# Kernel tuning notes

Hardware: AMD Instinct MI355X
Metric: run time of the kernel (lower is better)

## Reference

```python
import jax, jax.numpy as jnp
import numpy as np

N_NODES = 20000
N_EDGES = 320000
F_IN = 128
H = 4        # heads per layer
D = 128      # per-head hidden dim
NEG_SLOPE = 0.2


def setup_inputs() -> dict:
    key = jax.random.key(0)
    ks = jax.random.split(key, 14)
    s = 0.05
    inp = {
        "feats": jax.random.normal(ks[0], (N_NODES, F_IN), jnp.float32),
        "src": jax.random.randint(ks[1], (N_EDGES,), 0, N_NODES, jnp.int64),
        "dst": jax.random.randint(ks[2], (N_EDGES,), 0, N_NODES, jnp.int64),
        # layer 1: in F_IN -> H heads x D, flatten agg
        "W1": s * jax.random.normal(ks[3], (F_IN, H * D), jnp.float32),
        "al1": s * jax.random.normal(ks[4], (H, D), jnp.float32),
        "ar1": s * jax.random.normal(ks[5], (H, D), jnp.float32),
        "b1": jnp.zeros((H * D,), jnp.float32),
        # layer 2: in H*D -> H heads x D, mean agg
        "W2": s * jax.random.normal(ks[6], (H * D, H * D), jnp.float32),
        "al2": s * jax.random.normal(ks[7], (H, D), jnp.float32),
        "ar2": s * jax.random.normal(ks[8], (H, D), jnp.float32),
        "b2": jnp.zeros((H * D,), jnp.float32),
        # readout Linear(D, 1)
        "Wr": s * jax.random.normal(ks[9], (D, 1), jnp.float32),
        "br": jnp.zeros((1,), jnp.float32),
    }
    return inp


def _gat_conv(x, src, dst, W, al, ar, b, n_nodes):
    """dgl GATConv: per-head linear, edge softmax over incoming edges, scatter-sum."""
    h, d = al.shape
    z = (x @ W).reshape(n_nodes, h, d)                      # [N,H,D]
    el = jnp.einsum('nhd,hd->nh', z, al)                    # [N,H]
    er = jnp.einsum('nhd,hd->nh', z, ar)                    # [N,H]
    e = jax.nn.leaky_relu(el[src] + er[dst], NEG_SLOPE)     # [E,H]
    # numerically stable softmax grouped by destination node
    emax = jax.lax.stop_gradient(jax.ops.segment_max(e, dst, num_segments=n_nodes))
    a = jnp.exp(e - emax[dst])                              # [E,H]
    denom = jax.ops.segment_sum(a, dst, num_segments=n_nodes)
    alpha = a / jnp.maximum(denom[dst], 1e-9)               # [E,H]
    out = jax.ops.segment_sum(alpha[:, :, None] * z[src], dst, num_segments=n_nodes)
    return out + b.reshape(1, h, d)                         # [N,H,D]


def reference(feats, src, dst, W1, al1, ar1, b1, W2, al2, ar2, b2, Wr, br):
    n = feats.shape[0]
    h1 = _gat_conv(feats, src, dst, W1, al1, ar1, b1, n)    # [N,H,D]
    h1 = jax.nn.elu(h1.reshape(n, -1))                      # flatten heads -> [N,H*D]
    h2 = _gat_conv(h1, src, dst, W2, al2, ar2, b2, n)       # [N,H,D]
    h2 = h2.mean(axis=1)                                    # mean over heads -> [N,D]
    node_preds = h2 @ Wr + br                               # [N,1]
    return node_preds.sum(axis=0)                           # [1]
```

## Files before the change

### kernel.cpp

```cpp
#include <hip/hip_runtime.h>
#include <hip/hip_bf16.h>
#include <cstddef>

constexpr int NN = 20000;
constexpr int NE = 320000;
constexpr int NHEAD = 4;
constexpr int ND = 128;
constexpr int HD = 512;
constexpr int MPAD = 20096;
constexpr int SLOTS = 64;
constexpr float NEG_SLOPE = 0.2f;

using short8 = __attribute__((ext_vector_type(8))) short;
using f32x4 = __attribute__((ext_vector_type(4))) float;
using f32x2 = __attribute__((ext_vector_type(2))) float;

__device__ inline void gload16(const void* g, void* l) {
  __builtin_amdgcn_global_load_lds(
      (const __attribute__((address_space(1))) void*)g,
      (__attribute__((address_space(3))) void*)l, 16, 0, 0);
}

__device__ inline unsigned char f32_to_fp8(float v) {
  int pk = __builtin_amdgcn_cvt_pk_fp8_f32(v, v, 0, false);
  return (unsigned char)(pk & 0xff);
}

__device__ inline float fastrcp(float x) { return __builtin_amdgcn_rcpf(x); }

__device__ inline float fast_elu(float x) {
  return (x > 0.f) ? x : (__expf(x) - 1.0f);
}

constexpr int S0 = NN;
constexpr int S1 = S0 + MPAD * 128 / 4;
constexpr int S2 = S1 + 512 * 128;
constexpr int S3 = S2 + 12 * 512;
constexpr int S4 = S3 + 256;
__global__ __launch_bounds__(256) void prep_kernel(
    const float* __restrict__ feats, const float* __restrict__ W1,
    const float* __restrict__ W2, const float* __restrict__ al2,
    const float* __restrict__ ar2, const float* __restrict__ Wr,
    __hip_bfloat16* __restrict__ featsb, __hip_bfloat16* __restrict__ W1t,
    float* __restrict__ vcomb, float* __restrict__ partials,
    int* __restrict__ cnt) {
  int t = blockIdx.x * 256 + threadIdx.x;
  if (t < S0) {
    cnt[t] = 0;
  } else if (t < S1) {
    int u = (t - S0) * 4;
    float4 f = (u < NN * 128) ? *reinterpret_cast<const float4*>(&feats[u])
                              : make_float4(0.f, 0.f, 0.f, 0.f);
    __hip_bfloat162 o0 = __float22bfloat162_rn(make_float2(f.x, f.y));
    __hip_bfloat162 o1 = __float22bfloat162_rn(make_float2(f.z, f.w));
    uint2 pk;
    pk.x = *reinterpret_cast<unsigned int*>(&o0);
    pk.y = *reinterpret_cast<unsigned int*>(&o1);
    *reinterpret_cast<uint2*>(&featsb[u]) = pk;
  } else if (t < S2) {
    int u = t - S1;
    W1t[u] = __float2bfloat16(W1[(size_t)(u & 127) * 512 + (u >> 7)]);
  } else if (t < S3) {
    int u = t - S2;
    int v = u >> 9, k = u & 511;
    int h = (v < 4) ? v : (v < 8) ? v - 4 : v - 8;
    const float* vec = (v < 4) ? (al2 + h * 128)
                     : (v < 8) ? (ar2 + h * 128) : Wr;
    const float* wrow = W2 + (size_t)k * 512 + h * 128;
    float s = 0.f;
    for (int d = 0; d < 128; ++d) s += wrow[d] * vec[d];
    vcomb[u] = s;
  } else if (t < S4) {
    partials[t - S3] = 0.f;
  }
}

__global__ __launch_bounds__(256) void gemm1_kernel(
    const __hip_bfloat16* __restrict__ A,
    const __hip_bfloat16* __restrict__ Bt,
    unsigned char* __restrict__ C,
    const float* __restrict__ al, const float* __restrict__ ar,
    float* __restrict__ el, float* __restrict__ er,
    const int* __restrict__ src, const int* __restrict__ dst,
    int* __restrict__ cnt, int* __restrict__ src_perm) {
  constexpr int K = 128;
  __shared__ short As[128 * 32];
  __shared__ short Bs[128 * 32];
  __shared__ float elbuf[4][128];
  __shared__ float erbuf[4][128];
  int t = threadIdx.x;

  {
    int nth = gridDim.x * gridDim.y * 256;
    int gid = (blockIdx.y * gridDim.x + blockIdx.x) * 256 + t;
    for (int e = gid; e < NE; e += nth) {
      int d = dst[e];
      int p = atomicAdd(&cnt[d], 1);
      if (p < SLOTS) src_perm[d * SLOTS + p] = src[e];
    }
  }

  int lane = t & 63;
  int wave = t >> 6;
  int rowBase = blockIdx.x * 128;
  int head = blockIdx.y;
  int colBase = head * 128;
  int woffr = (wave & 1) * 64;
  int woffc = (wave >> 1) * 64;
  int mrow = lane & 15, quad = lane >> 4;

  f32x4 acc[4][4];
#pragma unroll
  for (int i = 0; i < 4; ++i)
#pragma unroll
    for (int j = 0; j < 4; ++j) acc[i][j] = (f32x4){0.f, 0.f, 0.f, 0.f};

  for (int k0 = 0; k0 < K; k0 += 32) {
#pragma unroll
    for (int p = 0; p < 2; ++p) {
      int f = p * 256 + wave * 64 + lane;
      int r = f >> 2, kc = f & 3;
      gload16(A + (size_t)(rowBase + r) * K + k0 + kc * 8,
              As + p * 2048 + wave * 512);
      gload16(Bt + (size_t)(colBase + r) * K + k0 + kc * 8,
              Bs + p * 2048 + wave * 512);
    }
    __syncthreads();
    short8 af[4], bfr[4];
#pragma unroll
    for (int i = 0; i < 4; ++i)
      af[i] = *(const short8*)&As[(woffr + i * 16 + mrow) * 32 + quad * 8];
#pragma unroll
    for (int j = 0; j < 4; ++j)
      bfr[j] = *(const short8*)&Bs[(woffc + j * 16 + mrow) * 32 + quad * 8];
#pragma unroll
    for (int i = 0; i < 4; ++i)
#pragma unroll
      for (int j = 0; j < 4; ++j)
        acc[i][j] = __builtin_amdgcn_mfma_f32_16x16x32_bf16(af[i], bfr[j], acc[i][j], 0, 0, 0);
    __syncthreads();
  }

#pragma unroll
  for (int i = 0; i < 4; ++i) {
#pragma unroll
    for (int j = 0; j < 4; ++j) {
      int col = colBase + woffc + j * 16 + mrow;
#pragma unroll
      for (int r = 0; r < 4; ++r) {
        int row = rowBase + woffr + i * 16 + quad * 4 + r;
        C[(size_t)row * HD + col] = f32_to_fp8(acc[i][j][r]);
      }
    }
  }

  float al_v[4], ar_v[4];
#pragma unroll
  for (int j = 0; j < 4; ++j) {
    int coll = woffc + j * 16 + mrow;
    al_v[j] = al[head * 128 + coll];
    ar_v[j] = ar[head * 128 + coll];
  }
#pragma unroll
  for (int i = 0; i < 4; ++i) {
#pragma unroll
    for (int r = 0; r < 4; ++r) {
      float pl = 0.f, pr = 0.f;
#pragma unroll
      for (int j = 0; j < 4; ++j) {
        float v = acc[i][j][r];
        pl += v * al_v[j];
        pr += v * ar_v[j];
      }
#pragma unroll
      for (int off = 1; off < 16; off <<= 1) {
        pl += __shfl_xor(pl, off);
        pr += __shfl_xor(pr, off);
      }
      if (mrow == 0) {
        int row128 = woffr + i * 16 + quad * 4 + r;
        elbuf[wave][row128] = pl;
        erbuf[wave][row128] = pr;
      }
    }
  }
  __syncthreads();
  if (t < 128) {
    int row = t;
    int w0 = (row < 64) ? 0 : 1;
    float ev = elbuf[w0][row] + elbuf[w0 + 2][row];
    float rv = erbuf[w0][row] + erbuf[w0 + 2][row];
    int gr = rowBase + row;
    if (gr < NN) {
      el[gr * 4 + head] = ev;
      er[gr * 4 + head] = rv;
    }
  }
}

struct __align__(8) APair { float a; int s; };
__global__ __launch_bounds__(256) void aggregate_kernel(
    const unsigned char* __restrict__ zf8,
    const int* __restrict__ cnt,
    const int* __restrict__ src_perm,
    const float* __restrict__ el,
    const float* __restrict__ er,
    const float* __restrict__ b1,
    const float* __restrict__ vcomb,
    float* __restrict__ el2,
    float* __restrict__ er2,
    float* __restrict__ q2) {
  __shared__ APair aslds[4][SLOTS][4];
  __shared__ float redbuf[4][12][4];
  int wv = __builtin_amdgcn_readfirstlane((int)(threadIdx.x >> 6));
  int n = blockIdx.x * 4 + wv;
  int lane = threadIdx.x & 63;
  int c = min(cnt[n], SLOTS);
  int base = n * SLOTS;

  {
    float4 er4 = *reinterpret_cast<const float4*>(&er[n * 4]);
    float a0 = 0.f, a1 = 0.f, a2 = 0.f, a3 = 0.f;
    int sv = 0;
    if (lane < c) {
      sv = src_perm[base + lane];
      float4 e4 = *reinterpret_cast<const float4*>(&el[sv * 4]);
      float x0 = e4.x + er4.x, x1 = e4.y + er4.y;
      float x2 = e4.z + er4.z, x3 = e4.w + er4.w;
      x0 = (x0 > 0.f) ? x0 : NEG_SLOPE * x0;
      x1 = (x1 > 0.f) ? x1 : NEG_SLOPE * x1;
      x2 = (x2 > 0.f) ? x2 : NEG_SLOPE * x2;
      x3 = (x3 > 0.f) ? x3 : NEG_SLOPE * x3;
      a0 = __expf(x0); a1 = __expf(x1); a2 = __expf(x2); a3 = __expf(x3);
    }
    float s0 = a0, s1 = a1, s2 = a2, s3 = a3;
#pragma unroll
    for (int off = 1; off < 64; off <<= 1) {
      s0 += __shfl_xor(s0, off);
      s1 += __shfl_xor(s1, off);
      s2 += __shfl_xor(s2, off);
      s3 += __shfl_xor(s3, off);
    }
    float i0 = fastrcp(fmaxf(s0, 1e-9f));
    float i1 = fastrcp(fmaxf(s1, 1e-9f));
    float i2 = fastrcp(fmaxf(s2, 1e-9f));
    float i3 = fastrcp(fmaxf(s3, 1e-9f));
    aslds[wv][lane][0] = {a0 * i0, sv};
    aslds[wv][lane][1] = {a1 * i1, sv};
    aslds[wv][lane][2] = {a2 * i2, sv};
    aslds[wv][lane][3] = {a3 * i3, sv};
  }

  int head = lane >> 4;
  float acc[8] = {};

#define EDGE_BODY(IDX)                                                         \
  {                                                                            \
    APair pr = aslds[wv][(IDX)][head];       \
    uint2 w = *reinterpret_cast<const uint2*>(zf8 + (size_t)pr.s * 512 + lane * 8); \
    f32x2 f0 = __builtin_amdgcn_cvt_pk_f32_fp8(w.x, false);                    \
    f32x2 f1 = __builtin_amdgcn_cvt_pk_f32_fp8(w.x, true);                     \
    f32x2 f2 = __builtin_amdgcn_cvt_pk_f32_fp8(w.y, false);                    \
    f32x2 f3 = __builtin_amdgcn_cvt_pk_f32_fp8(w.y, true);                     \
    acc[0] += pr.a * f0.x; acc[1] += pr.a * f0.y;                              \
    acc[2] += pr.a * f1.x; acc[3] += pr.a * f1.y;                              \
    acc[4] += pr.a * f2.x; acc[5] += pr.a * f2.y;                              \
    acc[6] += pr.a * f3.x; acc[7] += pr.a * f3.y;                              \
  }

  int i = 0;
  for (; i + 3 < c; i += 4) {
    EDGE_BODY(i)
    EDGE_BODY(i + 1)
    EDGE_BODY(i + 2)
    EDGE_BODY(i + 3)
  }
  for (; i < c; ++i) EDGE_BODY(i)
#undef EDGE_BODY

  float4 bA = *reinterpret_cast<const float4*>(&b1[lane * 8]);
  float4 bB = *reinterpret_cast<const float4*>(&b1[lane * 8 + 4]);
  float v[8];
  v[0] = fast_elu(acc[0] + bA.x); v[1] = fast_elu(acc[1] + bA.y);
  v[2] = fast_elu(acc[2] + bA.z); v[3] = fast_elu(acc[3] + bA.w);
  v[4] = fast_elu(acc[4] + bB.x); v[5] = fast_elu(acc[5] + bB.y);
  v[6] = fast_elu(acc[6] + bB.z); v[7] = fast_elu(acc[7] + bB.w);

  int li = lane & 15, g = lane >> 4;
#pragma unroll
  for (int vv = 0; vv < 12; ++vv) {
    const float* vb = vcomb + vv * 512 + lane * 8;
    float4 cA = *reinterpret_cast<const float4*>(vb);
    float4 cB = *reinterpret_cast<const float4*>(vb + 4);
    float p = v[0] * cA.x + v[1] * cA.y + v[2] * cA.z + v[3] * cA.w +
              v[4] * cB.x + v[5] * cB.y + v[6] * cB.z + v[7] * cB.w;
#pragma unroll
    for (int off = 1; off < 16; off <<= 1) p += __shfl_xor(p, off);
    if (li == 0) redbuf[wv][vv][g] = p;
  }
  if (lane < 12) {
    float s = redbuf[wv][lane][0] + redbuf[wv][lane][1] +
              redbuf[wv][lane][2] + redbuf[wv][lane][3];
    int h = lane & 3;
    float* dstp = (lane < 4) ? el2 : (lane < 8) ? er2 : q2;
    dstp[n * 4 + h] = s;
  }
}

__global__ __launch_bounds__(256) void attn_q_kernel(
    const int* __restrict__ src_perm,
    const int* __restrict__ cnt,
    const float* __restrict__ el,
    const float* __restrict__ er,
    const float* __restrict__ q,
    float* __restrict__ partials) {
  __shared__ float blk[4];
  int wv = __builtin_amdgcn_readfirstlane((int)(threadIdx.x >> 6));
  int n = blockIdx.x * 4 + wv;
  int lane = threadIdx.x & 63;
  int c = min(cnt[n], SLOTS);
  float4 er4 = *reinterpret_cast<const float4*>(&er[n * 4]);
  float a0 = 0.f, a1 = 0.f, a2 = 0.f, a3 = 0.f;
  int s = 0;
  if (lane < c) {
    s = src_perm[n * SLOTS + lane];
    float4 e4 = *reinterpret_cast<const float4*>(&el[s * 4]);
    float x0 = e4.x + er4.x, x1 = e4.y + er4.y;
    float x2 = e4.z + er4.z, x3 = e4.w + er4.w;
    x0 = (x0 > 0.f) ? x0 : NEG_SLOPE * x0;
    x1 = (x1 > 0.f) ? x1 : NEG_SLOPE * x1;
    x2 = (x2 > 0.f) ? x2 : NEG_SLOPE * x2;
    x3 = (x3 > 0.f) ? x3 : NEG_SLOPE * x3;
    a0 = __expf(x0); a1 = __expf(x1); a2 = __expf(x2); a3 = __expf(x3);
  }
  float s0 = a0, s1 = a1, s2 = a2, s3 = a3;
#pragma unroll
  for (int off = 1; off < 64; off <<= 1) {
    s0 += __shfl_xor(s0, off);
    s1 += __shfl_xor(s1, off);
    s2 += __shfl_xor(s2, off);
    s3 += __shfl_xor(s3, off);
  }
  float p = 0.f;
  if (lane < c) {
    float4 q4 = *reinterpret_cast<const float4*>(&q[s * 4]);
    p = (a0 * fastrcp(fmaxf(s0, 1e-9f))) * q4.x +
        (a1 * fastrcp(fmaxf(s1, 1e-9f))) * q4.y +
        (a2 * fastrcp(fmaxf(s2, 1e-9f))) * q4.z +
        (a3 * fastrcp(fmaxf(s3, 1e-9f))) * q4.w;
  }
#pragma unroll
  for (int off = 32; off > 0; off >>= 1) p += __shfl_down(p, off);
  if (lane == 0) blk[wv] = p;
  __syncthreads();
  if (threadIdx.x == 0) {
    atomicAdd(&partials[blockIdx.x & 255], blk[0] + blk[1] + blk[2] + blk[3]);
  }
}

__global__ __launch_bounds__(512) void final_kernel(
    const float* __restrict__ partials, const float* __restrict__ b2,
    const float* __restrict__ Wr, const float* __restrict__ br,
    float* __restrict__ out) {
  __shared__ float tmp[512];
  int t = threadIdx.x;
  float sum = (t < 256) ? partials[t] : 0.f;
  sum += (float)NN * b2[t] * Wr[t & 127];
  tmp[t] = sum;
  __syncthreads();
  for (int off = 256; off > 0; off >>= 1) {
    if (t < off) tmp[t] += tmp[t + off];
    __syncthreads();
  }
  if (t == 0) out[0] = 0.25f * tmp[0] + (float)NN * br[0];
}

extern "C" void kernel_launch(void* const* d_in, const int* in_sizes, int n_in,
                              void* d_out, int out_size, void* d_ws, size_t ws_size,
                              hipStream_t stream) {
  const float* feats = (const float*)d_in[0];
  const int* src = (const int*)d_in[1];
  const int* dst = (const int*)d_in[2];
  const float* W1 = (const float*)d_in[3];
  const float* al1 = (const float*)d_in[4];
  const float* ar1 = (const float*)d_in[5];
  const float* b1 = (const float*)d_in[6];
  const float* W2 = (const float*)d_in[7];
  const float* al2 = (const float*)d_in[8];
  const float* ar2 = (const float*)d_in[9];
  const float* b2 = (const float*)d_in[10];
  const float* Wr = (const float*)d_in[11];
  const float* br = (const float*)d_in[12];
  float* out = (float*)d_out;

  __hip_bfloat16* featsb = (__hip_bfloat16*)d_ws;
  unsigned char* zf8 = (unsigned char*)(featsb + (size_t)MPAD * 128);
  __hip_bfloat16* W1t = (__hip_bfloat16*)(zf8 + (size_t)MPAD * HD);
  float* vcomb = (float*)(W1t + 512 * 128);
  float* el1 = vcomb + 12 * 512;
  float* er1 = el1 + (size_t)NN * NHEAD;
  float* el2 = er1 + (size_t)NN * NHEAD;
  float* er2 = el2 + (size_t)NN * NHEAD;
  float* q2 = er2 + (size_t)NN * NHEAD;
  float* partials = q2 + (size_t)NN * NHEAD;
  int* cnt = (int*)(partials + 256 + 4);
  int* src_perm = cnt + NN;

  prep_kernel<<<(S4 + 255) / 256, 256, 0, stream>>>(
      feats, W1, W2, al2, ar2, Wr, featsb, W1t, vcomb, partials, cnt);

  dim3 gemm_grid(MPAD / 128, NHEAD);

  gemm1_kernel<<<gemm_grid, 256, 0, stream>>>(featsb, W1t, zf8, al1, ar1,
                                              el1, er1, src, dst, cnt, src_perm);

  aggregate_kernel<<<NN / 4, 256, 0, stream>>>(zf8, cnt, src_perm, el1, er1, b1,
                                               vcomb, el2, er2, q2);

  attn_q_kernel<<<NN / 4, 256, 0, stream>>>(src_perm, cnt, el2, er2, q2, partials);
  final_kernel<<<1, 512, 0, stream>>>(partials, b2, Wr, br, out);
}
```

Measured before the change: 170.8 us.

## Aggregate raw features before layer-1 projection, folding attention vectors into W1

Layer-1 attention logits are now computed from the 128-dim input features using precomputed W1·al1 and W1·ar1 vectors, so the full z = X·W1 projection is no longer needed before aggregation. Each node gathers its neighbours' bf16 input features (128 wide) weighted per head, writes a 4×128 aggregate, and only then runs a per-head GEMM with ELU and the layer-2 projections fused in its epilogue. This replaces an fp8 512-wide gather per edge with a bf16 128-wide gather, cutting gather traffic, at the cost of an extra kernel launch and an intermediate aggregate buffer. Numerics change slightly: fp8 storage of z is replaced by bf16 aggregates.

```diff
diff --git a/kernel.cpp b/kernel.cpp
--- a/kernel.cpp
+++ b/kernel.cpp
@@ -5,7 +5,6 @@
 constexpr int NN = 20000;
 constexpr int NE = 320000;
 constexpr int NHEAD = 4;
-constexpr int ND = 128;
 constexpr int HD = 512;
 constexpr int MPAD = 20096;
 constexpr int SLOTS = 64;
@@ -13,7 +12,6 @@
 
 using short8 = __attribute__((ext_vector_type(8))) short;
 using f32x4 = __attribute__((ext_vector_type(4))) float;
-using f32x2 = __attribute__((ext_vector_type(2))) float;
 
 __device__ inline void gload16(const void* g, void* l) {
   __builtin_amdgcn_global_load_lds(
@@ -21,11 +19,6 @@
       (__attribute__((address_space(3))) void*)l, 16, 0, 0);
 }
 
-__device__ inline unsigned char f32_to_fp8(float v) {
-  int pk = __builtin_amdgcn_cvt_pk_fp8_f32(v, v, 0, false);
-  return (unsigned char)(pk & 0xff);
-}
-
 __device__ inline float fastrcp(float x) { return __builtin_amdgcn_rcpf(x); }
 
 __device__ inline float fast_elu(float x) {
@@ -33,24 +26,26 @@
 }
 
 constexpr int S0 = NN;
-constexpr int S1 = S0 + MPAD * 128 / 4;
+constexpr int S1 = S0 + NN * 128 / 4;
 constexpr int S2 = S1 + 512 * 128;
 constexpr int S3 = S2 + 12 * 512;
-constexpr int S4 = S3 + 256;
+constexpr int S4 = S3 + 1024;
+constexpr int S5 = S4 + 256;
 __global__ __launch_bounds__(256) void prep_kernel(
     const float* __restrict__ feats, const float* __restrict__ W1,
-    const float* __restrict__ W2, const float* __restrict__ al2,
+    const float* __restrict__ W2, const float* __restrict__ al1,
+    const float* __restrict__ ar1, const float* __restrict__ al2,
     const float* __restrict__ ar2, const float* __restrict__ Wr,
     __hip_bfloat16* __restrict__ featsb, __hip_bfloat16* __restrict__ W1t,
-    float* __restrict__ vcomb, float* __restrict__ partials,
+    float* __restrict__ vcomb, float* __restrict__ wl1t,
+    float* __restrict__ wr1t, float* __restrict__ partials,
     int* __restrict__ cnt) {
   int t = blockIdx.x * 256 + threadIdx.x;
   if (t < S0) {
     cnt[t] = 0;
   } else if (t < S1) {
     int u = (t - S0) * 4;
-    float4 f = (u < NN * 128) ? *reinterpret_cast<const float4*>(&feats[u])
-                              : make_float4(0.f, 0.f, 0.f, 0.f);
+    float4 f = *reinterpret_cast<const float4*>(&feats[u]);
     __hip_bfloat162 o0 = __float22bfloat162_rn(make_float2(f.x, f.y));
     __hip_bfloat162 o1 = __float22bfloat162_rn(make_float2(f.z, f.w));
     uint2 pk;
@@ -71,159 +66,83 @@
     for (int d = 0; d < 128; ++d) s += wrow[d] * vec[d];
     vcomb[u] = s;
   } else if (t < S4) {
-    partials[t - S3] = 0.f;
-  }
-}
-
-__global__ __launch_bounds__(256) void gemm1_kernel(
-    const __hip_bfloat16* __restrict__ A,
-    const __hip_bfloat16* __restrict__ Bt,
-    unsigned char* __restrict__ C,
-    const float* __restrict__ al, const float* __restrict__ ar,
-    float* __restrict__ el, float* __restrict__ er,
+    int u = t - S3;
+    int d = u >> 3, rem = u & 7, h = rem >> 1, sel = rem & 1;
+    const float* vec = (sel ? ar1 : al1) + h * 128;
+    const float* wrow = W1 + (size_t)d * 512 + h * 128;
+    float s = 0.f;
+    for (int dd = 0; dd < 128; ++dd) s += wrow[dd] * vec[dd];
+    (sel ? wr1t : wl1t)[d * 4 + h] = s;
+  } else if (t < S5) {
+    partials[t - S4] = 0.f;
+  }
+}
+
+__global__ __launch_bounds__(256) void fill_logits_kernel(
     const int* __restrict__ src, const int* __restrict__ dst,
-    int* __restrict__ cnt, int* __restrict__ src_perm) {
-  constexpr int K = 128;
-  __shared__ short As[128 * 32];
-  __shared__ short Bs[128 * 32];
-  __shared__ float elbuf[4][128];
-  __shared__ float erbuf[4][128];
+    int* __restrict__ cnt, int* __restrict__ src_perm,
+    const __hip_bfloat16* __restrict__ featsb,
+    const float* __restrict__ wl1t, const float* __restrict__ wr1t,
+    float* __restrict__ el1, float* __restrict__ er1) {
   int t = threadIdx.x;
-
   {
-    int nth = gridDim.x * gridDim.y * 256;
-    int gid = (blockIdx.y * gridDim.x + blockIdx.x) * 256 + t;
+    int nth = gridDim.x * 256;
+    int gid = blockIdx.x * 256 + t;
     for (int e = gid; e < NE; e += nth) {
       int d = dst[e];
       int p = atomicAdd(&cnt[d], 1);
       if (p < SLOTS) src_perm[d * SLOTS + p] = src[e];
     }
   }
-
-  int lane = t & 63;
-  int wave = t >> 6;
-  int rowBase = blockIdx.x * 128;
-  int head = blockIdx.y;
-  int colBase = head * 128;
-  int woffr = (wave & 1) * 64;
-  int woffc = (wave >> 1) * 64;
-  int mrow = lane & 15, quad = lane >> 4;
-
-  f32x4 acc[4][4];
-#pragma unroll
-  for (int i = 0; i < 4; ++i)
-#pragma unroll
-    for (int j = 0; j < 4; ++j) acc[i][j] = (f32x4){0.f, 0.f, 0.f, 0.f};
-
-  for (int k0 = 0; k0 < K; k0 += 32) {
-#pragma unroll
-    for (int p = 0; p < 2; ++p) {
-      int f = p * 256 + wave * 64 + lane;
-      int r = f >> 2, kc = f & 3;
-      gload16(A + (size_t)(rowBase + r) * K + k0 + kc * 8,
-              As + p * 2048 + wave * 512);
-      gload16(Bt + (size_t)(colBase + r) * K + k0 + kc * 8,
-              Bs + p * 2048 + wave * 512);
-    }
-    __syncthreads();
-    short8 af[4], bfr[4];
-#pragma unroll
-    for (int i = 0; i < 4; ++i)
-      af[i] = *(const short8*)&As[(woffr + i * 16 + mrow) * 32 + quad * 8];
-#pragma unroll
-    for (int j = 0; j < 4; ++j)
-      bfr[j] = *(const short8*)&Bs[(woffc + j * 16 + mrow) * 32 + quad * 8];
-#pragma unroll
-    for (int i = 0; i < 4; ++i)
-#pragma unroll
-      for (int j = 0; j < 4; ++j)
-        acc[i][j] = __builtin_amdgcn_mfma_f32_16x16x32_bf16(af[i], bfr[j], acc[i][j], 0, 0, 0);
-    __syncthreads();
-  }
-
-#pragma unroll
-  for (int i = 0; i < 4; ++i) {
-#pragma unroll
-    for (int j = 0; j < 4; ++j) {
-      int col = colBase + woffc + j * 16 + mrow;
-#pragma unroll
-      for (int r = 0; r < 4; ++r) {
-        int row = rowBase + woffr + i * 16 + quad * 4 + r;
-        C[(size_t)row * HD + col] = f32_to_fp8(acc[i][j][r]);
-      }
-    }
-  }
-
-  float al_v[4], ar_v[4];
-#pragma unroll
-  for (int j = 0; j < 4; ++j) {
-    int coll = woffc + j * 16 + mrow;
-    al_v[j] = al[head * 128 + coll];
-    ar_v[j] = ar[head * 128 + coll];
-  }
-#pragma unroll
-  for (int i = 0; i < 4; ++i) {
-#pragma unroll
-    for (int r = 0; r < 4; ++r) {
-      float pl = 0.f, pr = 0.f;
-#pragma unroll
-      for (int j = 0; j < 4; ++j) {
-        float v = acc[i][j][r];
-        pl += v * al_v[j];
-        pr += v * ar_v[j];
-      }
-#pragma unroll
-      for (int off = 1; off < 16; off <<= 1) {
-        pl += __shfl_xor(pl, off);
-        pr += __shfl_xor(pr, off);
-      }
-      if (mrow == 0) {
-        int row128 = woffr + i * 16 + quad * 4 + r;
-        elbuf[wave][row128] = pl;
-        erbuf[wave][row128] = pr;
-      }
-    }
-  }
-  __syncthreads();
-  if (t < 128) {
-    int row = t;
-    int w0 = (row < 64) ? 0 : 1;
-    float ev = elbuf[w0][row] + elbuf[w0 + 2][row];
-    float rv = erbuf[w0][row] + erbuf[w0 + 2][row];
-    int gr = rowBase + row;
-    if (gr < NN) {
-      el[gr * 4 + head] = ev;
-      er[gr * 4 + head] = rv;
-    }
-  }
-}
-
-struct __align__(8) APair { float a; int s; };
-__global__ __launch_bounds__(256) void aggregate_kernel(
-    const unsigned char* __restrict__ zf8,
-    const int* __restrict__ cnt,
-    const int* __restrict__ src_perm,
-    const float* __restrict__ el,
-    const float* __restrict__ er,
-    const float* __restrict__ b1,
-    const float* __restrict__ vcomb,
-    float* __restrict__ el2,
-    float* __restrict__ er2,
-    float* __restrict__ q2) {
-  __shared__ APair aslds[4][SLOTS][4];
-  __shared__ float redbuf[4][12][4];
+  int wv = t >> 6, lane = t & 63;
+  int n = blockIdx.x * 4 + wv;
+  unsigned int uu = *reinterpret_cast<const unsigned int*>(
+      &featsb[(size_t)n * 128 + 2 * lane]);
+  __hip_bfloat162 ub = *reinterpret_cast<__hip_bfloat162*>(&uu);
+  float2 f = __bfloat1622float2(ub);
+  float4 wlA = *reinterpret_cast<const float4*>(&wl1t[lane * 8]);
+  float4 wlB = *reinterpret_cast<const float4*>(&wl1t[lane * 8 + 4]);
+  float4 wrA = *reinterpret_cast<const float4*>(&wr1t[lane * 8]);
+  float4 wrB = *reinterpret_cast<const float4*>(&wr1t[lane * 8 + 4]);
+  float p0 = f.x * wlA.x + f.y * wlB.x;
+  float p1 = f.x * wlA.y + f.y * wlB.y;
+  float p2 = f.x * wlA.z + f.y * wlB.z;
+  float p3 = f.x * wlA.w + f.y * wlB.w;
+  float p4 = f.x * wrA.x + f.y * wrB.x;
+  float p5 = f.x * wrA.y + f.y * wrB.y;
+  float p6 = f.x * wrA.z + f.y * wrB.z;
+  float p7 = f.x * wrA.w + f.y * wrB.w;
+#pragma unroll
+  for (int off = 1; off < 64; off <<= 1) {
+    p0 += __shfl_xor(p0, off); p1 += __shfl_xor(p1, off);
+    p2 += __shfl_xor(p2, off); p3 += __shfl_xor(p3, off);
+    p4 += __shfl_xor(p4, off); p5 += __shfl_xor(p5, off);
+    p6 += __shfl_xor(p6, off); p7 += __shfl_xor(p7, off);
+  }
+  if (lane == 0) {
+    *reinterpret_cast<float4*>(&el1[n * 4]) = make_float4(p0, p1, p2, p3);
+    *reinterpret_cast<float4*>(&er1[n * 4]) = make_float4(p4, p5, p6, p7);
+  }
+}
+
+__global__ __launch_bounds__(256) void gather_kernel(
+    const __hip_bfloat16* __restrict__ featsb,
+    const int* __restrict__ cnt, const int* __restrict__ src_perm,
+    const float* __restrict__ el, const float* __restrict__ er,
+    __hip_bfloat16* __restrict__ aggb) {
+  __shared__ float4 alph[4][SLOTS];
+  __shared__ int srcb[4][SLOTS];
   int wv = __builtin_amdgcn_readfirstlane((int)(threadIdx.x >> 6));
   int n = blockIdx.x * 4 + wv;
   int lane = threadIdx.x & 63;
   int c = min(cnt[n], SLOTS);
-  int base = n * SLOTS;
 
   {
     float4 er4 = *reinterpret_cast<const float4*>(&er[n * 4]);
     float a0 = 0.f, a1 = 0.f, a2 = 0.f, a3 = 0.f;
     int sv = 0;
     if (lane < c) {
-      sv = src_perm[base + lane];
+      sv = src_perm[n * SLOTS + lane];
       float4 e4 = *reinterpret_cast<const float4*>(&el[sv * 4]);
       float x0 = e4.x + er4.x, x1 = e4.y + er4.y;
       float x2 = e4.z + er4.z, x3 = e4.w + er4.w;
@@ -245,65 +164,152 @@
     float i1 = fastrcp(fmaxf(s1, 1e-9f));
     float i2 = fastrcp(fmaxf(s2, 1e-9f));
     float i3 = fastrcp(fmaxf(s3, 1e-9f));
-    aslds[wv][lane][0] = {a0 * i0, sv};
-    aslds[wv][lane][1] = {a1 * i1, sv};
-    aslds[wv][lane][2] = {a2 * i2, sv};
-    aslds[wv][lane][3] = {a3 * i3, sv};
-  }
-
-  int head = lane >> 4;
-  float acc[8] = {};
-
-#define EDGE_BODY(IDX)                                                         \
+    alph[wv][lane] = make_float4(a0 * i0, a1 * i1, a2 * i2, a3 * i3);
+    srcb[wv][lane] = sv;
+  }
+
+  float acc[4][2] = {};
+
+#define EB(IDX)                                                                \
   {                                                                            \
-    APair pr = aslds[wv][(IDX)][head];       \
-    uint2 w = *reinterpret_cast<const uint2*>(zf8 + (size_t)pr.s * 512 + lane * 8); \
-    f32x2 f0 = __builtin_amdgcn_cvt_pk_f32_fp8(w.x, false);                    \
-    f32x2 f1 = __builtin_amdgcn_cvt_pk_f32_fp8(w.x, true);                     \
-    f32x2 f2 = __builtin_amdgcn_cvt_pk_f32_fp8(w.y, false);                    \
-    f32x2 f3 = __builtin_amdgcn_cvt_pk_f32_fp8(w.y, true);                     \
-    acc[0] += pr.a * f0.x; acc[1] += pr.a * f0.y;                              \
-    acc[2] += pr.a * f1.x; acc[3] += pr.a * f1.y;                              \
-    acc[4] += pr.a * f2.x; acc[5] += pr.a * f2.y;                              \
-    acc[6] += pr.a * f3.x; acc[7] += pr.a * f3.y;                              \
+    float4 a4 = alph[wv][(IDX)];                                               \
+    int s = srcb[wv][(IDX)];                                                   \
+    unsigned int uu = *reinterpret_cast<const unsigned int*>(                  \
+        &featsb[(size_t)s * 128 + 2 * lane]);                                  \
+    __hip_bfloat162 ub = *reinterpret_cast<__hip_bfloat162*>(&uu);             \
+    float2 f = __bfloat1622float2(ub);                                         \
+    acc[0][0] += a4.x * f.x; acc[0][1] += a4.x * f.y;                          \
+    acc[1][0] += a4.y * f.x; acc[1][1] += a4.y * f.y;                          \
+    acc[2][0] += a4.z * f.x; acc[2][1] += a4.z * f.y;                          \
+    acc[3][0] += a4.w * f.x; acc[3][1] += a4.w * f.y;                          \
   }
 
   int i = 0;
   for (; i + 3 < c; i += 4) {
-    EDGE_BODY(i)
-    EDGE_BODY(i + 1)
-    EDGE_BODY(i + 2)
-    EDGE_BODY(i + 3)
-  }
-  for (; i < c; ++i) EDGE_BODY(i)
-#undef EDGE_BODY
-
-  float4 bA = *reinterpret_cast<const float4*>(&b1[lane * 8]);
-  float4 bB = *reinterpret_cast<const float4*>(&b1[lane * 8 + 4]);
-  float v[8];
-  v[0] = fast_elu(acc[0] + bA.x); v[1] = fast_elu(acc[1] + bA.y);
-  v[2] = fast_elu(acc[2] + bA.z); v[3] = fast_elu(acc[3] + bA.w);
-  v[4] = fast_elu(acc[4] + bB.x); v[5] = fast_elu(acc[5] + bB.y);
-  v[6] = fast_elu(acc[6] + bB.z); v[7] = fast_elu(acc[7] + bB.w);
-
-  int li = lane & 15, g = lane >> 4;
-#pragma unroll
-  for (int vv = 0; vv < 12; ++vv) {
-    const float* vb = vcomb + vv * 512 + lane * 8;
-    float4 cA = *reinterpret_cast<const float4*>(vb);
-    float4 cB = *reinterpret_cast<const float4*>(vb + 4);
-    float p = v[0] * cA.x + v[1] * cA.y + v[2] * cA.z + v[3] * cA.w +
-              v[4] * cB.x + v[5] * cB.y + v[6] * cB.z + v[7] * cB.w;
-#pragma unroll
-    for (int off = 1; off < 16; off <<= 1) p += __shfl_xor(p, off);
-    if (li == 0) redbuf[wv][vv][g] = p;
-  }
-  if (lane < 12) {
-    float s = redbuf[wv][lane][0] + redbuf[wv][lane][1] +
-              redbuf[wv][lane][2] + redbuf[wv][lane][3];
-    int h = lane & 3;
-    float* dstp = (lane < 4) ? el2 : (lane < 8) ? er2 : q2;
-    dstp[n * 4 + h] = s;
+    EB(i) EB(i + 1) EB(i + 2) EB(i + 3)
+  }
+  for (; i < c; ++i) EB(i)
+#undef EB
+
+  size_t obase = (size_t)n * HD + 2 * lane;
+#pragma unroll
+  for (int h = 0; h < 4; ++h) {
+    __hip_bfloat162 o = __float22bfloat162_rn(make_float2(acc[h][0], acc[h][1]));
+    *reinterpret_cast<unsigned int*>(&aggb[obase + h * 128]) =
+        *reinterpret_cast<unsigned int*>(&o);
+  }
+}
+
+__global__ __launch_bounds__(256) void h1_gemm_kernel(
+    const __hip_bfloat16* __restrict__ A,
+    const __hip_bfloat16* __restrict__ Bt,
+    const float* __restrict__ b1,
+    const float* __restrict__ vcomb,
+    float* __restrict__ el2, float* __restrict__ er2,
+    float* __restrict__ q2) {
+  __shared__ short As[64 * 32];
+  __shared__ short Bs[128 * 32];
+  __shared__ float vc[12 * 512];
+  __shared__ float redbuf[64][12][2];
+  int t = threadIdx.x;
+  for (int idx = t; idx < 12 * 512; idx += 256) vc[idx] = vcomb[idx];
+  int lane = t & 63, wave = t >> 6;
+  int rowBase = blockIdx.x * 64;
+  int woffr = (wave & 1) * 32;
+  int woffc = (wave >> 1) * 64;
+  int ch = wave >> 1;
+  int mrow = lane & 15, quad = lane >> 4;
+  float keep[8] = {0.f, 0.f, 0.f, 0.f, 0.f, 0.f, 0.f, 0.f};
+  __syncthreads();
+
+  for (int head = 0; head < 4; ++head) {
+    f32x4 acc[2][4];
+#pragma unroll
+    for (int i = 0; i < 2; ++i)
+#pragma unroll
+      for (int j = 0; j < 4; ++j) acc[i][j] = (f32x4){0.f, 0.f, 0.f, 0.f};
+
+    for (int k0 = 0; k0 < 128; k0 += 32) {
+      {
+        int f = wave * 64 + lane;
+        int r = f >> 2, kc = f & 3;
+        gload16(A + (size_t)(rowBase + r) * HD + head * 128 + k0 + kc * 8,
+                As + wave * 512);
+      }
+#pragma unroll
+      for (int p = 0; p < 2; ++p) {
+        int f = p * 256 + wave * 64 + lane;
+        int r = f >> 2, kc = f & 3;
+        gload16(Bt + (size_t)(head * 128 + r) * 128 + k0 + kc * 8,
+                Bs + p * 2048 + wave * 512);
+      }
+      __syncthreads();
+      short8 af[2], bfr[4];
+#pragma unroll
+      for (int i = 0; i < 2; ++i)
+        af[i] = *(const short8*)&As[(woffr + i * 16 + mrow) * 32 + quad * 8];
+#pragma unroll
+      for (int j = 0; j < 4; ++j)
+        bfr[j] = *(const short8*)&Bs[(woffc + j * 16 + mrow) * 32 + quad * 8];
+#pragma unroll
+      for (int i = 0; i < 2; ++i)
+#pragma unroll
+        for (int j = 0; j < 4; ++j)
+          acc[i][j] = __builtin_amdgcn_mfma_f32_16x16x32_bf16(af[i], bfr[j],
+                                                              acc[i][j], 0, 0, 0);
+      __syncthreads();
+    }
+
+    float b1g[4];
+#pragma unroll
+    for (int j = 0; j < 4; ++j)
+      b1g[j] = b1[head * 128 + woffc + j * 16 + mrow];
+#pragma unroll
+    for (int i = 0; i < 2; ++i)
+#pragma unroll
+      for (int j = 0; j < 4; ++j)
+#pragma unroll
+        for (int r = 0; r < 4; ++r)
+          acc[i][j][r] = fast_elu(acc[i][j][r] + b1g[j]);
+
+#pragma unroll
+    for (int vv = 0; vv < 12; ++vv) {
+      float vc4[4];
+#pragma unroll
+      for (int j = 0; j < 4; ++j)
+        vc4[j] = vc[vv * 512 + head * 128 + woffc + j * 16 + mrow];
+#pragma unroll
+      for (int i = 0; i < 2; ++i)
+#pragma unroll
+        for (int r = 0; r < 4; ++r) {
+          float p = acc[i][0][r] * vc4[0] + acc[i][1][r] * vc4[1] +
+                    acc[i][2][r] * vc4[2] + acc[i][3][r] * vc4[3];
+          p += __shfl_xor(p, 1);
+          p += __shfl_xor(p, 2);
+          p += __shfl_xor(p, 4);
+          p += __shfl_xor(p, 8);
+          if (mrow == vv) keep[i * 4 + r] += p;
+        }
+    }
+  }
+
+  if (mrow < 12) {
+#pragma unroll
+    for (int i = 0; i < 2; ++i)
+#pragma unroll
+      for (int r = 0; r < 4; ++r)
+        redbuf[woffr + i * 16 + quad * 4 + r][mrow][ch] = keep[i * 4 + r];
+  }
+  __syncthreads();
+  for (int idx = t; idx < 64 * 12; idx += 256) {
+    int node = idx / 12;
+    int vv = idx - node * 12;
+    float s = redbuf[node][vv][0] + redbuf[node][vv][1];
+    int n = rowBase + node;
+    if (n < NN) {
+      float* dp = (vv < 4) ? el2 : (vv < 8) ? er2 : q2;
+      dp[(size_t)n * 4 + (vv & 3)] = s;
+    }
   }
 }
 
@@ -394,29 +400,34 @@
   float* out = (float*)d_out;
 
   __hip_bfloat16* featsb = (__hip_bfloat16*)d_ws;
-  unsigned char* zf8 = (unsigned char*)(featsb + (size_t)MPAD * 128);
-  __hip_bfloat16* W1t = (__hip_bfloat16*)(zf8 + (size_t)MPAD * HD);
+  __hip_bfloat16* aggb = featsb + (size_t)NN * 128;
+  __hip_bfloat16* W1t = aggb + (size_t)MPAD * HD;
   float* vcomb = (float*)(W1t + 512 * 128);
-  float* el1 = vcomb + 12 * 512;
+  float* wl1t = vcomb + 12 * 512;
+  float* wr1t = wl1t + 512;
+  float* el1 = wr1t + 512;
   float* er1 = el1 + (size_t)NN * NHEAD;
   float* el2 = er1 + (size_t)NN * NHEAD;
   float* er2 = el2 + (size_t)NN * NHEAD;
   float* q2 = er2 + (size_t)NN * NHEAD;
   float* partials = q2 + (size_t)NN * NHEAD;
-  int* cnt = (int*)(partials + 256 + 4);
+  int* cnt = (int*)(partials + 256);
   int* src_perm = cnt + NN;
 
-  prep_kernel<<<(S4 + 255) / 256, 256, 0, stream>>>(
-      feats, W1, W2, al2, ar2, Wr, featsb, W1t, vcomb, partials, cnt);
-
-  dim3 gemm_grid(MPAD / 128, NHEAD);
-
-  gemm1_kernel<<<gemm_grid, 256, 0, stream>>>(featsb, W1t, zf8, al1, ar1,
-                                              el1, er1, src, dst, cnt, src_perm);
-
-  aggregate_kernel<<<NN / 4, 256, 0, stream>>>(zf8, cnt, src_perm, el1, er1, b1,
-                                               vcomb, el2, er2, q2);
-
-  attn_q_kernel<<<NN / 4, 256, 0, stream>>>(src_perm, cnt, el2, er2, q2, partials);
+  prep_kernel<<<(S5 + 255) / 256, 256, 0, stream>>>(
+      feats, W1, W2, al1, ar1, al2, ar2, Wr, featsb, W1t, vcomb, wl1t, wr1t,
+      partials, cnt);
+
+  fill_logits_kernel<<<NN / 4, 256, 0, stream>>>(
+      src, dst, cnt, src_perm, featsb, wl1t, wr1t, el1, er1);
+
+  gather_kernel<<<NN / 4, 256, 0, stream>>>(featsb, cnt, src_perm, el1, er1,
+                                            aggb);
+
+  h1_gemm_kernel<<<MPAD / 64, 256, 0, stream>>>(aggb, W1t, b1, vcomb, el2,
+                                                er2, q2);
+
+  attn_q_kernel<<<NN / 4, 256, 0, stream>>>(src_perm, cnt, el2, er2, q2,
+                                            partials);
   final_kernel<<<1, 512, 0, stream>>>(partials, b2, Wr, br, out);
 }
```

After: 268.6 us. 1.57x slower.
